# Kernel tuning notes

Measured on AMD Instinct MI355X. Metric: run time of the kernel, lower is better.

## Reference

```python
import jax, jax.numpy as jnp
import numpy as np

N, F_IN, F_OUT = 8192, 512, 256


def setup_inputs() -> dict:
    key = jax.random.key(0)
    k1, k2, k3, k4 = jax.random.split(key, 4)
    x = jax.random.normal(k1, (N, F_IN), dtype=jnp.float32)
    adj = jax.random.randint(k2, (N, N), 0, 2, dtype=jnp.int32)
    # xavier_uniform with gain=1.414
    limW = 1.414 * np.sqrt(6.0 / (F_IN + F_OUT))
    W = jax.random.uniform(k3, (F_IN, F_OUT), dtype=jnp.float32, minval=-limW, maxval=limW)
    lima = 1.414 * np.sqrt(6.0 / (2 * F_OUT + 1))
    a = jax.random.uniform(k4, (2 * F_OUT, 1), dtype=jnp.float32, minval=-lima, maxval=lima)
    return {"x": x, "adj": adj, "W": W, "a": a}


def reference(x, adj, W, a):
    # h = x @ W : [N, F_out]
    h = x @ W
    f_out = h.shape[1]
    # additive score a^T [h_i ; h_j] is separable: (h @ a_l)_i + (h @ a_r)_j
    f_src = h @ a[:f_out, 0]   # [N]
    f_dst = h @ a[f_out:, 0]   # [N]
    e = jax.nn.leaky_relu(f_src[:, None] + f_dst[None, :], negative_slope=0.2)  # [N, N]
    e = jnp.where(adj > 0, e, jnp.float32(-9e15))
    attention = jax.nn.softmax(e, axis=1)  # row-wise over neighbors
    # dropout(p=0.6) is identity in eval mode
    h_prime = attention @ h  # [N, F_out]
    return h_prime
```

## Files before the change

kernel.cpp:

```cpp
#include <hip/hip_runtime.h>
#include <hip/hip_bf16.h>

#define NN 8192
#define FIN 512
#define FOUT 256
#define JTILE 64

typedef __attribute__((ext_vector_type(8))) short short8;
typedef __attribute__((ext_vector_type(4))) float float4v;
typedef __attribute__((ext_vector_type(16))) float float16v;

#if __has_builtin(__builtin_amdgcn_exp2f)
#define EXP2(x) __builtin_amdgcn_exp2f(x)
#else
#define EXP2(x) exp2f(x)
#endif

__device__ __forceinline__ short f2bf(float f) {
    union { float f; unsigned u; } v; v.f = f;
    unsigned r = (v.u + 0x7FFFu + ((v.u >> 16) & 1u)) >> 16;
    return (short)r;
}

__global__ __launch_bounds__(256) void wt_kernel(const float* __restrict__ W,
                                                 short* __restrict__ Wt) {
    __shared__ short tile[32][33];
    int tx = threadIdx.x & 31, ty = threadIdx.x >> 5;
    int k0 = blockIdx.x * 32, n0 = blockIdx.y * 32;
#pragma unroll
    for (int r = 0; r < 32; r += 8)
        tile[ty + r][tx] = f2bf(W[(size_t)(k0 + ty + r) * FOUT + n0 + tx]);
    __syncthreads();
#pragma unroll
    for (int r = 0; r < 32; r += 8)
        Wt[(size_t)(n0 + ty + r) * FIN + k0 + tx] = tile[tx][ty + r];
}

__global__ __launch_bounds__(256) void h_kernel(const float* __restrict__ x,
                                                const short* __restrict__ Wt,
                                                const float* __restrict__ a,
                                                short* __restrict__ h_t,
                                                float* __restrict__ f_src,
                                                float* __restrict__ f_dst) {
    int wave = (blockIdx.x << 2) + (threadIdx.x >> 6);
    int lane = threadIdx.x & 63;
    int m0 = (wave & 511) << 4;
    int n0 = (wave >> 9) << 6;
    int lr = lane & 15, lq = lane >> 4;

    const float* xrow = x + (size_t)(m0 + lr) * FIN + lq * 8;
    const short* wbase = Wt + (size_t)(n0 + lr) * FIN + lq * 8;

    float4v acc[4] = {};
    for (int k0 = 0; k0 < FIN; k0 += 32) {
        float4v xa = *(const float4v*)(xrow + k0);
        float4v xb = *(const float4v*)(xrow + k0 + 4);
        short8 av;
        av[0] = f2bf(xa[0]); av[1] = f2bf(xa[1]); av[2] = f2bf(xa[2]); av[3] = f2bf(xa[3]);
        av[4] = f2bf(xb[0]); av[5] = f2bf(xb[1]); av[6] = f2bf(xb[2]); av[7] = f2bf(xb[3]);
#pragma unroll
        for (int ct = 0; ct < 4; ct++) {
            short8 bv = *(const short8*)(wbase + (size_t)ct * 16 * FIN + k0);
            acc[ct] = __builtin_amdgcn_mfma_f32_16x16x32_bf16(av, bv, acc[ct], 0, 0, 0);
        }
    }
    float s_part[4] = {0.f, 0.f, 0.f, 0.f};
    float d_part[4] = {0.f, 0.f, 0.f, 0.f};
#pragma unroll
    for (int ct = 0; ct < 4; ct++) {
        int n = n0 + ct * 16 + lr;
        float al = a[n], ar = a[FOUT + n];
#pragma unroll
        for (int reg = 0; reg < 4; reg++) {
            float hv = acc[ct][reg];
            s_part[reg] = fmaf(hv, al, s_part[reg]);
            d_part[reg] = fmaf(hv, ar, d_part[reg]);
            h_t[(size_t)n * NN + (m0 + lq * 4 + reg)] = f2bf(hv);
        }
    }
#pragma unroll
    for (int off = 1; off < 16; off <<= 1) {
#pragma unroll
        for (int reg = 0; reg < 4; reg++) {
            s_part[reg] += __shfl_xor(s_part[reg], off);
            d_part[reg] += __shfl_xor(d_part[reg], off);
        }
    }
    const float LOG2E = 1.4426950408889634f;
    if (lr == 0) {
#pragma unroll
        for (int reg = 0; reg < 4; reg++) {
            atomicAdd(&f_src[m0 + lq * 4 + reg], s_part[reg] * LOG2E);
            atomicAdd(&f_dst[m0 + lq * 4 + reg], d_part[reg] * LOG2E);
        }
    }
}

__global__ __launch_bounds__(256, 3) void gat_kernel(const int* __restrict__ adj,
                                                     const short* __restrict__ h_t,
                                                     const float* __restrict__ f_src,
                                                     const float* __restrict__ f_dst,
                                                     float* __restrict__ Opart,
                                                     float* __restrict__ lpart,
                                                     int jlen) {
    __shared__ short Pt[2][64 * 64];
    __shared__ float Fd[2][64];

    const int t = threadIdx.x;
    const int i0 = blockIdx.x * 64;
    const int slice = blockIdx.y;
    const int jbase = slice * jlen;

    const int prow = t >> 2, pjq = t & 3;
    const int lane = t & 63, w = t >> 6;
    const int l31 = lane & 31, lq = lane >> 5;
    const int wn0 = w * 64;

    const float fs = f_src[i0 + prow];
    const int* adjRow = adj + (size_t)(i0 + prow) * NN + jbase;
    const short* hb0 = h_t + (size_t)(wn0 + l31) * NN + jbase + lq * 8;
    const short* hb1 = hb0 + (size_t)32 * NN;

    float16v acc00 = {}, acc01 = {}, acc10 = {}, acc11 = {};
    float lp = 0.f;

    if (t < 16) *(float4*)&Fd[0][t * 4] = *(const float4*)(f_dst + jbase + t * 4);
    int4 av0 = *(const int4*)(adjRow + pjq * 16);
    int4 av1 = *(const int4*)(adjRow + pjq * 16 + 4);
    int4 av2 = *(const int4*)(adjRow + pjq * 16 + 8);
    int4 av3 = *(const int4*)(adjRow + pjq * 16 + 12);
    __syncthreads();

    int buf = 0;
    const int pswz = (prow & 7) << 4;
    const int rswz = (l31 & 7) << 4;
    const int wb = prow * 128 + pjq * 32;

    for (int jo = 0; jo < jlen; jo += JTILE) {
        short8 b0[4], b1[4];
#pragma unroll
        for (int kk = 0; kk < 4; kk++) {
            b0[kk] = *(const short8*)(hb0 + jo + kk * 16);
            b1[kk] = *(const short8*)(hb1 + jo + kk * 16);
        }
        const bool more = (jo + JTILE) < jlen;
        const int* ap = adjRow + (more ? jo + JTILE : 0) + pjq * 16;
        int4 an0 = *(const int4*)(ap);
        int4 an1 = *(const int4*)(ap + 4);
        int4 an2 = *(const int4*)(ap + 8);
        int4 an3 = *(const int4*)(ap + 12);

        {
            const float4v fd0 = *(const float4v*)&Fd[buf][pjq * 16];
            const float4v fd1 = *(const float4v*)&Fd[buf][pjq * 16 + 4];
            const float4v fd2 = *(const float4v*)&Fd[buf][pjq * 16 + 8];
            const float4v fd3 = *(const float4v*)&Fd[buf][pjq * 16 + 12];
            short8 pbl, pbh;
#define PEL(A, FDV, DST, IDX)                              \
            {                                              \
                float y = fs + (FDV);                      \
                y = fmaxf(y, 0.2f * y);                    \
                float p = ((A) != 0) ? EXP2(y) : 0.f;      \
                lp += p;                                   \
                DST[IDX] = f2bf(p);                        \
            }
            PEL(av0.x, fd0[0], pbl, 0) PEL(av0.y, fd0[1], pbl, 1)
            PEL(av0.z, fd0[2], pbl, 2) PEL(av0.w, fd0[3], pbl, 3)
            PEL(av1.x, fd1[0], pbl, 4) PEL(av1.y, fd1[1], pbl, 5)
            PEL(av1.z, fd1[2], pbl, 6) PEL(av1.w, fd1[3], pbl, 7)
            PEL(av2.x, fd2[0], pbh, 0) PEL(av2.y, fd2[1], pbh, 1)
            PEL(av2.z, fd2[2], pbh, 2) PEL(av2.w, fd2[3], pbh, 3)
            PEL(av3.x, fd3[0], pbh, 4) PEL(av3.y, fd3[1], pbh, 5)
            PEL(av3.z, fd3[2], pbh, 6) PEL(av3.w, fd3[3], pbh, 7)
#undef PEL
            char* pbuf = (char*)&Pt[buf][0];
            *(short8*)(pbuf + (wb ^ pswz)) = pbl;
            *(short8*)(pbuf + ((wb + 16) ^ pswz)) = pbh;
        }
        if (t < 16) {
            float4 fdn = *(const float4*)(f_dst + jbase + (more ? jo + JTILE : 0) + t * 4);
            *(float4*)&Fd[buf ^ 1][t * 4] = fdn;
        }

        asm volatile("s_waitcnt lgkmcnt(0)\n\ts_barrier" ::: "memory");

        {
            const char* pbuf = (const char*)&Pt[buf][0];
            const int ra = l31 * 128 + lq * 16;
#pragma unroll
            for (int kk = 0; kk < 4; kk++) {
                short8 a0 = *(const short8*)(pbuf + ((ra + kk * 32) ^ rswz));
                short8 a1 = *(const short8*)(pbuf + ((ra + 4096 + kk * 32) ^ rswz));
                acc00 = __builtin_amdgcn_mfma_f32_32x32x16_bf16(a0, b0[kk], acc00, 0, 0, 0);
                acc01 = __builtin_amdgcn_mfma_f32_32x32x16_bf16(a0, b1[kk], acc01, 0, 0, 0);
                acc10 = __builtin_amdgcn_mfma_f32_32x32x16_bf16(a1, b0[kk], acc10, 0, 0, 0);
                acc11 = __builtin_amdgcn_mfma_f32_32x32x16_bf16(a1, b1[kk], acc11, 0, 0, 0);
            }
        }
        av0 = an0; av1 = an1; av2 = an2; av3 = an3;
        buf ^= 1;
    }

    lp += __shfl_xor(lp, 1);
    lp += __shfl_xor(lp, 2);
    if (pjq == 0) lpart[slice * NN + i0 + prow] = lp;

    float* obase = Opart + ((size_t)slice * NN + i0) * FOUT;
#pragma unroll
    for (int rt = 0; rt < 2; rt++) {
#pragma unroll
        for (int nt = 0; nt < 2; nt++) {
            const float16v& av = rt == 0 ? (nt == 0 ? acc00 : acc01) : (nt == 0 ? acc10 : acc11);
#pragma unroll
            for (int reg = 0; reg < 16; reg++) {
                int row = rt * 32 + (reg & 3) + 8 * (reg >> 2) + 4 * lq;
                int n = wn0 + nt * 32 + l31;
                obase[(size_t)row * FOUT + n] = av[reg];
            }
        }
    }
}

__global__ __launch_bounds__(256) void combine_kernel(const float* __restrict__ Opart,
                                                      const float* __restrict__ lpart,
                                                      float* __restrict__ out, int slices) {
    int i = blockIdx.x, n = threadIdx.x;
    float o = 0.f, l = 0.f;
    for (int s = 0; s < slices; s++) {
        o += Opart[((size_t)s * NN + i) * FOUT + n];
        l += lpart[s * NN + i];
    }
    out[(size_t)i * FOUT + n] = o / l;
}

extern "C" void kernel_launch(void* const* d_in, const int* in_sizes, int n_in,
                              void* d_out, int out_size, void* d_ws, size_t ws_size,
                              hipStream_t stream) {
    const float* x   = (const float*)d_in[0];
    const int*   adj = (const int*)d_in[1];
    const float* W   = (const float*)d_in[2];
    const float* a   = (const float*)d_in[3];
    float* out = (float*)d_out;

    char* ws = (char*)d_ws;
    short* h_t   = (short*)ws;
    short* Wt    = (short*)(ws + (4u << 20));
    float* f_src = (float*)(ws + (4u << 20) + (256u << 10));
    float* f_dst = (float*)(ws + (4u << 20) + (288u << 10));
    float* lpart = (float*)(ws + (4u << 20) + (320u << 10));
    float* Opart = (float*)(ws + (5u << 20));

    const size_t OSLICE = (size_t)NN * FOUT * 4;
    int slices = 1;
    if (ws_size >= (size_t)(5u << 20) + 8 * OSLICE) slices = 8;
    else if (ws_size >= (size_t)(5u << 20) + 4 * OSLICE) slices = 4;
    else if (ws_size >= (size_t)(5u << 20) + 2 * OSLICE) slices = 2;
    int jlen = NN / slices;

    hipMemsetAsync(f_src, 0, 2 * NN * sizeof(float), stream);
    wt_kernel<<<dim3(FIN / 32, FOUT / 32), 256, 0, stream>>>(W, Wt);
    h_kernel<<<512, 256, 0, stream>>>(x, Wt, a, h_t, f_src, f_dst);
    gat_kernel<<<dim3(NN / 64, slices), 256, 0, stream>>>(adj, h_t, f_src, f_dst,
                                                          Opart, lpart, jlen);
    combine_kernel<<<NN, 256, 0, stream>>>(Opart, lpart, out, slices);
}
```

Baseline: 468.4 us.

## Restructure GAT attention loop with windowed f_dst staging, packed bf16 conversion, nontemporal IO

Rewrites the main gat_kernel loop. f_dst is now staged in a 2048-entry LDS window, replacing the per-tile double-buffered copy. The loop is unrolled into even/odd subtiles with ping-pong adjacency registers. Other changes: hardware packed bf16 conversion (v_cvt_pk_bf16_f32) instead of manual rounding, nontemporal loads for adjacency and nontemporal stores for partial outputs, s_setprio around the MFMA section, and occupancy raised from 3 to 4 blocks. The aim is less per-tile synchronization and VALU overhead, with more latency hiding. The risks are higher register pressure from the larger occupancy target and the extra LDS used by the window.

```diff
diff --git a/kernel.cpp b/kernel.cpp
--- a/kernel.cpp
+++ b/kernel.cpp
@@ -5,9 +5,11 @@
 #define FIN 512
 #define FOUT 256
 #define JTILE 64
+#define FDWIN 2048
 
 typedef __attribute__((ext_vector_type(8))) short short8;
 typedef __attribute__((ext_vector_type(4))) float float4v;
+typedef __attribute__((ext_vector_type(4))) int int4v;
 typedef __attribute__((ext_vector_type(16))) float float16v;
 
 #if __has_builtin(__builtin_amdgcn_exp2f)
@@ -20,6 +22,12 @@
     union { float f; unsigned u; } v; v.f = f;
     unsigned r = (v.u + 0x7FFFu + ((v.u >> 16) & 1u)) >> 16;
     return (short)r;
+}
+
+__device__ __forceinline__ unsigned cvt_pk_bf16(float lo, float hi) {
+    unsigned r;
+    asm("v_cvt_pk_bf16_f32 %0, %1, %2" : "=v"(r) : "v"(lo), "v"(hi));
+    return r;
 }
 
 __global__ __launch_bounds__(256) void wt_kernel(const float* __restrict__ W,
@@ -96,7 +104,7 @@
     }
 }
 
-__global__ __launch_bounds__(256, 3) void gat_kernel(const int* __restrict__ adj,
+__global__ __launch_bounds__(256, 4) void gat_kernel(const int* __restrict__ adj,
                                                      const short* __restrict__ h_t,
                                                      const float* __restrict__ f_src,
                                                      const float* __restrict__ f_dst,
@@ -104,7 +112,7 @@
                                                      float* __restrict__ lpart,
                                                      int jlen) {
     __shared__ short Pt[2][64 * 64];
-    __shared__ float Fd[2][64];
+    __shared__ float Fdall[FDWIN];
 
     const int t = threadIdx.x;
     const int i0 = blockIdx.x * 64;
@@ -112,9 +120,9 @@
     const int jbase = slice * jlen;
 
     const int prow = t >> 2, pjq = t & 3;
-    const int lane = t & 63, w = t >> 6;
+    const int lane = t & 63, wv = t >> 6;
     const int l31 = lane & 31, lq = lane >> 5;
-    const int wn0 = w * 64;
+    const int wn0 = wv * 64;
 
     const float fs = f_src[i0 + prow];
     const int* adjRow = adj + (size_t)(i0 + prow) * NN + jbase;
@@ -124,82 +132,94 @@
     float16v acc00 = {}, acc01 = {}, acc10 = {}, acc11 = {};
     float lp = 0.f;
 
-    if (t < 16) *(float4*)&Fd[0][t * 4] = *(const float4*)(f_dst + jbase + t * 4);
-    int4 av0 = *(const int4*)(adjRow + pjq * 16);
-    int4 av1 = *(const int4*)(adjRow + pjq * 16 + 4);
-    int4 av2 = *(const int4*)(adjRow + pjq * 16 + 8);
-    int4 av3 = *(const int4*)(adjRow + pjq * 16 + 12);
-    __syncthreads();
-
-    int buf = 0;
     const int pswz = (prow & 7) << 4;
     const int rswz = (l31 & 7) << 4;
     const int wb = prow * 128 + pjq * 32;
-
-    for (int jo = 0; jo < jlen; jo += JTILE) {
-        short8 b0[4], b1[4];
-#pragma unroll
-        for (int kk = 0; kk < 4; kk++) {
-            b0[kk] = *(const short8*)(hb0 + jo + kk * 16);
-            b1[kk] = *(const short8*)(hb1 + jo + kk * 16);
-        }
-        const bool more = (jo + JTILE) < jlen;
-        const int* ap = adjRow + (more ? jo + JTILE : 0) + pjq * 16;
-        int4 an0 = *(const int4*)(ap);
-        int4 an1 = *(const int4*)(ap + 4);
-        int4 an2 = *(const int4*)(ap + 8);
-        int4 an3 = *(const int4*)(ap + 12);
-
+    const int ra = l31 * 128 + lq * 16;
+
+    int4v avE0, avE1, avE2, avE3, avO0, avO1, avO2, avO3;
+
+#define PEL(A, FI, I) { float y_ = fs + fdp[FI]; y_ = fmaxf(y_, 0.2f * y_); \
+                        pv[I] = ((A) != 0) ? EXP2(y_) : 0.f; }
+
+#define SUBTILE(BUF, R0, R1, R2, R3, W0, W1, W2, W3, JOB, JON)                          \
+    {                                                                                   \
+        short8 b0_[4], b1_[4];                                                          \
+        _Pragma("unroll")                                                               \
+        for (int kk = 0; kk < 4; kk++) {                                                \
+            b0_[kk] = *(const short8*)(hb0 + (JOB) + kk * 16);                          \
+            b1_[kk] = *(const short8*)(hb1 + (JOB) + kk * 16);                          \
+        }                                                                               \
+        {             \
+            const int4v* ap_ = (const int4v*)(adjRow + (JON) + pjq * 16);               \
+            W0 = __builtin_nontemporal_load(ap_);                                       \
+            W1 = __builtin_nontemporal_load(ap_ + 1);                                   \
+            W2 = __builtin_nontemporal_load(ap_ + 2);                                   \
+            W3 = __builtin_nontemporal_load(ap_ + 3);                                   \
+        }                                                                               \
+        {                                                                               \
+            const float* fdp = &Fdall[(JOB) - w0 + pjq * 16];                           \
+            float pv[16];                                                               \
+            PEL(R0[0], 0, 0)   PEL(R0[1], 1, 1)   PEL(R0[2], 2, 2)   PEL(R0[3], 3, 3)  \
+            PEL(R1[0], 4, 4)   PEL(R1[1], 5, 5)   PEL(R1[2], 6, 6)   PEL(R1[3], 7, 7)  \
+            PEL(R2[0], 8, 8)   PEL(R2[1], 9, 9)   PEL(R2[2], 10, 10) PEL(R2[3], 11, 11)\
+            PEL(R3[0], 12, 12) PEL(R3[1], 13, 13) PEL(R3[2], 14, 14) PEL(R3[3], 15, 15)\
+            lp += ((pv[0] + pv[1]) + (pv[2] + pv[3])) + ((pv[4] + pv[5]) + (pv[6] + pv[7])) \
+                + ((pv[8] + pv[9]) + (pv[10] + pv[11])) + ((pv[12] + pv[13]) + (pv[14] + pv[15])); \
+            int4v lov, hiv;                                                             \
+            lov[0] = (int)cvt_pk_bf16(pv[0], pv[1]);                                    \
+            lov[1] = (int)cvt_pk_bf16(pv[2], pv[3]);                                    \
+            lov[2] = (int)cvt_pk_bf16(pv[4], pv[5]);                                    \
+            lov[3] = (int)cvt_pk_bf16(pv[6], pv[7]);                                    \
+            hiv[0] = (int)cvt_pk_bf16(pv[8], pv[9]);                                    \
+            hiv[1] = (int)cvt_pk_bf16(pv[10], pv[11]);                                  \
+            hiv[2] = (int)cvt_pk_bf16(pv[12], pv[13]);                                  \
+            hiv[3] = (int)cvt_pk_bf16(pv[14], pv[15]);                                  \
+            char* pbuf_ = (char*)&Pt[BUF][0];                                           \
+            *(int4v*)(pbuf_ + (wb ^ pswz)) = lov;                                       \
+            *(int4v*)(pbuf_ + ((wb + 16) ^ pswz)) = hiv;                                \
+        }                                                                               \
+        asm volatile("s_waitcnt lgkmcnt(0)\n\ts_barrier" ::: "memory");                 \
+        __builtin_amdgcn_s_setprio(1);                                                  \
+        {                                                                               \
+            const char* pbuf_ = (const char*)&Pt[BUF][0];                               \
+            _Pragma("unroll")                                                           \
+            for (int kk = 0; kk < 4; kk++) {                                            \
+                short8 a0_ = *(const short8*)(pbuf_ + ((ra + kk * 32) ^ rswz));         \
+                short8 a1_ = *(const short8*)(pbuf_ + ((ra + 4096 + kk * 32) ^ rswz));  \
+                acc00 = __builtin_amdgcn_mfma_f32_32x32x16_bf16(a0_, b0_[kk], acc00, 0, 0, 0); \
+                acc01 = __builtin_amdgcn_mfma_f32_32x32x16_bf16(a0_, b1_[kk], acc01, 0, 0, 0); \
+                acc10 = __builtin_amdgcn_mfma_f32_32x32x16_bf16(a1_, b0_[kk], acc10, 0, 0, 0); \
+                acc11 = __builtin_amdgcn_mfma_f32_32x32x16_bf16(a1_, b1_[kk], acc11, 0, 0, 0); \
+            }                                                                           \
+        }                                                                               \
+        __builtin_amdgcn_s_setprio(0);                                                  \
+    }
+
+    for (int w0 = 0; w0 < jlen; w0 += FDWIN) {
+        const int wl = (jlen - w0 < FDWIN) ? (jlen - w0) : FDWIN;
+        if (t * 8 < wl) {
+            *(float4v*)&Fdall[t * 8]     = *(const float4v*)(f_dst + jbase + w0 + t * 8);
+            *(float4v*)&Fdall[t * 8 + 4] = *(const float4v*)(f_dst + jbase + w0 + t * 8 + 4);
+        }
+        __syncthreads();
         {
-            const float4v fd0 = *(const float4v*)&Fd[buf][pjq * 16];
-            const float4v fd1 = *(const float4v*)&Fd[buf][pjq * 16 + 4];
-            const float4v fd2 = *(const float4v*)&Fd[buf][pjq * 16 + 8];
-            const float4v fd3 = *(const float4v*)&Fd[buf][pjq * 16 + 12];
-            short8 pbl, pbh;
-#define PEL(A, FDV, DST, IDX)                              \
-            {                                              \
-                float y = fs + (FDV);                      \
-                y = fmaxf(y, 0.2f * y);                    \
-                float p = ((A) != 0) ? EXP2(y) : 0.f;      \
-                lp += p;                                   \
-                DST[IDX] = f2bf(p);                        \
-            }
-            PEL(av0.x, fd0[0], pbl, 0) PEL(av0.y, fd0[1], pbl, 1)
-            PEL(av0.z, fd0[2], pbl, 2) PEL(av0.w, fd0[3], pbl, 3)
-            PEL(av1.x, fd1[0], pbl, 4) PEL(av1.y, fd1[1], pbl, 5)
-            PEL(av1.z, fd1[2], pbl, 6) PEL(av1.w, fd1[3], pbl, 7)
-            PEL(av2.x, fd2[0], pbh, 0) PEL(av2.y, fd2[1], pbh, 1)
-            PEL(av2.z, fd2[2], pbh, 2) PEL(av2.w, fd2[3], pbh, 3)
-            PEL(av3.x, fd3[0], pbh, 4) PEL(av3.y, fd3[1], pbh, 5)
-            PEL(av3.z, fd3[2], pbh, 6) PEL(av3.w, fd3[3], pbh, 7)
+            const int4v* ap_ = (const int4v*)(adjRow + w0 + pjq * 16);
+            avE0 = __builtin_nontemporal_load(ap_);
+            avE1 = __builtin_nontemporal_load(ap_ + 1);
+            avE2 = __builtin_nontemporal_load(ap_ + 2);
+            avE3 = __builtin_nontemporal_load(ap_ + 3);
+        }
+        for (int jo = w0; jo < w0 + wl; jo += 2 * JTILE) {
+            SUBTILE(0, avE0, avE1, avE2, avE3, avO0, avO1, avO2, avO3,
+                    jo, jo + JTILE)
+            const int jnn = (jo + 2 * JTILE < w0 + wl) ? (jo + 2 * JTILE) : w0;
+            SUBTILE(1, avO0, avO1, avO2, avO3, avE0, avE1, avE2, avE3,
+                    jo + JTILE, jnn)
+        }
+    }
+#undef SUBTILE
 #undef PEL
-            char* pbuf = (char*)&Pt[buf][0];
-            *(short8*)(pbuf + (wb ^ pswz)) = pbl;
-            *(short8*)(pbuf + ((wb + 16) ^ pswz)) = pbh;
-        }
-        if (t < 16) {
-            float4 fdn = *(const float4*)(f_dst + jbase + (more ? jo + JTILE : 0) + t * 4);
-            *(float4*)&Fd[buf ^ 1][t * 4] = fdn;
-        }
-
-        asm volatile("s_waitcnt lgkmcnt(0)\n\ts_barrier" ::: "memory");
-
-        {
-            const char* pbuf = (const char*)&Pt[buf][0];
-            const int ra = l31 * 128 + lq * 16;
-#pragma unroll
-            for (int kk = 0; kk < 4; kk++) {
-                short8 a0 = *(const short8*)(pbuf + ((ra + kk * 32) ^ rswz));
-                short8 a1 = *(const short8*)(pbuf + ((ra + 4096 + kk * 32) ^ rswz));
-                acc00 = __builtin_amdgcn_mfma_f32_32x32x16_bf16(a0, b0[kk], acc00, 0, 0, 0);
-                acc01 = __builtin_amdgcn_mfma_f32_32x32x16_bf16(a0, b1[kk], acc01, 0, 0, 0);
-                acc10 = __builtin_amdgcn_mfma_f32_32x32x16_bf16(a1, b0[kk], acc10, 0, 0, 0);
-                acc11 = __builtin_amdgcn_mfma_f32_32x32x16_bf16(a1, b1[kk], acc11, 0, 0, 0);
-            }
-        }
-        av0 = an0; av1 = an1; av2 = an2; av3 = an3;
-        buf ^= 1;
-    }
 
     lp += __shfl_xor(lp, 1);
     lp += __shfl_xor(lp, 2);
@@ -215,7 +235,7 @@
             for (int reg = 0; reg < 16; reg++) {
                 int row = rt * 32 + (reg & 3) + 8 * (reg >> 2) + 4 * lq;
                 int n = wn0 + nt * 32 + l31;
-                obase[(size_t)row * FOUT + n] = av[reg];
+                __builtin_nontemporal_store(av[reg], &obase[(size_t)row * FOUT + n]);
             }
         }
     }
```

Result: slower. 920.2 us (+96.5%).
